# Kernel optimization log

Measured on AMD Instinct MI355X. Metric: run time of the kernel, lower is better.

The kernel has to match this reference:

```python
import jax, jax.numpy as jnp
import numpy as np

PADDING = 1
STRIDE = 1

def setup_inputs() -> dict:
    key = jax.random.key(0)
    k1, k2 = jax.random.split(key)
    x = jax.random.normal(k1, (32, 64, 64, 64), dtype=jnp.float32)
    # kaiming_normal fan_out, relu: std = sqrt(2 / (out_ch * k * k))
    fan_out = 128 * 3 * 3
    std = np.sqrt(2.0 / fan_out).astype(np.float32)
    weight = jax.random.normal(k2, (128, 64, 3, 3), dtype=jnp.float32) * std
    bias = jnp.zeros((128,), dtype=jnp.float32)
    return {"x": x, "weight": weight, "bias": bias}

def reference(x, weight, bias):
    # Faithful to the unfold+multiply+sum path, which computes a standard
    # cross-correlation conv2d (torch conv semantics) with stride/padding.
    out = jax.lax.conv_general_dilated(
        x, weight,
        window_strides=(STRIDE, STRIDE),
        padding=[(PADDING, PADDING), (PADDING, PADDING)],
        dimension_numbers=("NCHW", "OIHW", "NCHW"),
    )
    return out + bias[None, :, None, None]
```

## Files before the change

kernel.cpp:

```cpp
#include <hip/hip_runtime.h>


typedef short short8 __attribute__((ext_vector_type(8)));
typedef float f32x4  __attribute__((ext_vector_type(4)));

static __device__ __forceinline__ unsigned short f2bf(float f) {
    unsigned int u = __float_as_uint(f);
    u = (u + 0x7FFFu + ((u >> 16) & 1u)) >> 16;
    return (unsigned short)u;
}
static __device__ __forceinline__ unsigned int pk2(float lo, float hi) {
    return (unsigned int)f2bf(lo) | ((unsigned int)f2bf(hi) << 16);
}

__global__ __launch_bounds__(256)
void prep_x(const float* __restrict__ x, unsigned short* __restrict__ xT)
{
    __shared__ float T[64][65];
    const int h = blockIdx.x, n = blockIdx.y, tid = threadIdx.x;
    const size_t nbase = (size_t)n * 262144 + (size_t)h * 64;
    #pragma unroll
    for (int i = 0; i < 16; ++i) {
        int idx = tid + i * 256;
        int ci = idx >> 6, w = idx & 63;
        T[ci][w] = x[nbase + (size_t)ci * 4096 + w];
    }
    __syncthreads();
    const int w = tid >> 2, cg = tid & 3;
    unsigned int pk[8];
    #pragma unroll
    for (int k = 0; k < 8; ++k)
        pk[k] = pk2(T[cg * 16 + 2 * k][w], T[cg * 16 + 2 * k + 1][w]);
    unsigned short* dst = xT + (((size_t)n * 64 + h) * 64 + w) * 64 + cg * 16;
    uint4 a; a.x = pk[0]; a.y = pk[1]; a.z = pk[2]; a.w = pk[3];
    uint4 b; b.x = pk[4]; b.y = pk[5]; b.z = pk[6]; b.w = pk[7];
    *(uint4*)(dst)     = a;
    *(uint4*)(dst + 8) = b;
}

__global__ __launch_bounds__(256)
void prep_w(const float* __restrict__ w, unsigned short* __restrict__ wT)
{
    int t = blockIdx.x * 256 + threadIdx.x;
    if (t >= 128 * 576) return;
    int co = t / 576, r = t - co * 576;
    int p = r >> 6, ci = r & 63;
    wT[t] = f2bf(w[(size_t)(co * 64 + ci) * 9 + p]);
}

#define XBUF 50688
#define WBUF 8192
#define TOTAL_LDS (XBUF + 2*WBUF)

__global__ __launch_bounds__(256, 2)
void conv_mfma3(const unsigned short* __restrict__ xT,
                const unsigned short* __restrict__ wT,
                const float* __restrict__ bias,
                float* __restrict__ out)
{
    extern __shared__ __align__(16) char lds[];
    char* wl = lds + XBUF;

    const int tid  = threadIdx.x;
    const int cb   = blockIdx.x;
    const int h0   = blockIdx.y * 4;
    const int n    = blockIdx.z;
    const int wrow = tid >> 6;
    const int lane = tid & 63;
    const int l15  = lane & 15, l4 = lane >> 4;

    const unsigned short* xTn = xT + (size_t)n * 262144;
    const unsigned short* wTb = wT + (size_t)cb * 64 * 576;

    const int wco = tid >> 3, wg = tid & 7;
    const int wds0 = wco * 128 + ((wg ^ (wco & 7)) * 16);
    const int wds1 = wds0 + 32 * 128;
    const unsigned short* wsrc0 = wTb + wco * 576 + wg * 8;
    const unsigned short* wsrc1 = wTb + (wco + 32) * 576 + wg * 8;

    f32x4 breg[4];
    #pragma unroll
    for (int mf = 0; mf < 4; ++mf)
        breg[mf] = *(const f32x4*)(bias + cb * 64 + mf * 16 + l4 * 4);

    {
        uint4 xreg[13];
        #pragma unroll
        for (int k = 0; k < 13; ++k) {
            int G = tid + k * 256;
            if (k < 12 || tid < 96) {
                int hp = G / 528, rem = G - hp * 528;
                int wp = rem >> 3, g = rem & 7;
                int gh = h0 + hp - 1, gw = wp - 1;
                uint4 v; v.x = v.y = v.z = v.w = 0u;
                if ((unsigned)gh < 64u && (unsigned)gw < 64u)
                    v = *(const uint4*)(xTn + ((gh * 64 + gw) * 64 + g * 8));
                xreg[k] = v;
            }
        }
        uint4 w0a = *(const uint4*)(wsrc0);
        uint4 w0b = *(const uint4*)(wsrc1);
        #pragma unroll
        for (int k = 0; k < 13; ++k) {
            int G = tid + k * 256;
            if (k < 12 || tid < 96) {
                int hp = G / 528, rem = G - hp * 528;
                int wp = rem >> 3, g = rem & 7;
                *(uint4*)(lds + (hp * 66 + wp) * 128 + ((g ^ (wp & 7)) * 16)) = xreg[k];
            }
        }
        *(uint4*)(wl + wds0) = w0a;
        *(uint4*)(wl + wds1) = w0b;
    }
    __syncthreads();

    f32x4 acc[4][4];
    #pragma unroll
    for (int mf = 0; mf < 4; ++mf)
        #pragma unroll
        for (int nf = 0; nf < 4; ++nf)
            acc[mf][nf] = (f32x4)0.0f;

    #pragma unroll
    for (int p = 0; p < 9; ++p) {
        const char* wbr = wl + ((p & 1) ? WBUF : 0);
        char*       wbw = wl + ((p & 1) ? 0 : WBUF);
        const int kh = p / 3, kw = p - kh * 3;

        uint4 nw0, nw1;
        if (p < 8) {
            nw0 = *(const uint4*)(wsrc0 + (p + 1) * 64);
            nw1 = *(const uint4*)(wsrc1 + (p + 1) * 64);
        }

        #pragma unroll
        for (int c = 0; c < 2; ++c) {
            short8 Af[4], Bf[4];
            #pragma unroll
            for (int mf = 0; mf < 4; ++mf) {
                const int co = mf * 16 + l15;
                Af[mf] = *(const short8*)(wbr + co * 128 + (((c * 4 + l4) ^ (co & 7)) * 16));
            }
            #pragma unroll
            for (int nf = 0; nf < 4; ++nf) {
                const int hp = wrow + kh;
                const int wp = nf * 16 + l15 + kw;
                Bf[nf] = *(const short8*)(lds + (hp * 66 + wp) * 128 + (((c * 4 + l4) ^ (wp & 7)) * 16));
            }
            #pragma unroll
            for (int mf = 0; mf < 4; ++mf)
                #pragma unroll
                for (int nf = 0; nf < 4; ++nf)
                    acc[mf][nf] = __builtin_amdgcn_mfma_f32_16x16x32_bf16(
                        Af[mf], Bf[nf], acc[mf][nf], 0, 0, 0);
        }

        if (p < 8) {
            *(uint4*)(wbw + wds0) = nw0;
            *(uint4*)(wbw + wds1) = nw1;
            __syncthreads();
        }
    }

    {
        const int h = h0 + wrow;
        #pragma unroll
        for (int mf = 0; mf < 4; ++mf) {
            #pragma unroll
            for (int r = 0; r < 4; ++r) {
                const int co = cb * 64 + mf * 16 + l4 * 4 + r;
                float* orow = out + (((size_t)n * 128 + co) * 64 + h) * 64;
                const float bv = breg[mf][r];
                #pragma unroll
                for (int nf = 0; nf < 4; ++nf)
                    orow[nf * 16 + l15] = acc[mf][nf][r] + bv;
            }
        }
    }
}

__global__ __launch_bounds__(256, 4)
void conv2d_f32_tiled(const float* __restrict__ x,
                      const float* __restrict__ wgt,
                      const float* __restrict__ bias,
                      float* __restrict__ out)
{
    __shared__ float Xlds[8][10][66];
    __shared__ float Wlds[32][72];
    const int tid = threadIdx.x;
    const int co0 = blockIdx.x * 32, h0 = blockIdx.y * 8, n = blockIdx.z;
    const int tco = tid >> 6, lane = tid & 63;
    float acc[8][8];
    #pragma unroll
    for (int i = 0; i < 8; ++i)
        #pragma unroll
        for (int j = 0; j < 8; ++j) acc[i][j] = 0.0f;
    for (int cc = 0; cc < 8; ++cc) {
        const int ci0 = cc * 8;
        for (int idx = tid; idx < 8 * 10 * 66; idx += 256) {
            const int ww = idx % 66, t = idx / 66, hh = t % 10, ci = t / 10;
            const int gh = h0 + hh - 1, gw = ww - 1;
            float v = 0.0f;
            if ((unsigned)gh < 64u && (unsigned)gw < 64u)
                v = x[(((size_t)n * 64 + ci0 + ci) * 64 + gh) * 64 + gw];
            Xlds[ci][hh][ww] = v;
        }
        for (int idx = tid; idx < 32 * 72; idx += 256) {
            const int r = idx % 72, co = idx / 72;
            Wlds[co][r] = wgt[(size_t)(co0 + co) * 576 + ci0 * 9 + r];
        }
        __syncthreads();
        for (int ci = 0; ci < 8; ++ci)
            #pragma unroll
            for (int kh = 0; kh < 3; ++kh)
                #pragma unroll
                for (int kw = 0; kw < 3; ++kw) {
                    float wv[8];
                    #pragma unroll
                    for (int i = 0; i < 8; ++i) wv[i] = Wlds[tco * 8 + i][ci * 9 + kh * 3 + kw];
                    #pragma unroll
                    for (int j = 0; j < 8; ++j) {
                        const float xv = Xlds[ci][j + kh][lane + kw];
                        #pragma unroll
                        for (int i = 0; i < 8; ++i) acc[i][j] = fmaf(wv[i], xv, acc[i][j]);
                    }
                }
        __syncthreads();
    }
    #pragma unroll
    for (int i = 0; i < 8; ++i) {
        const int co = co0 + tco * 8 + i;
        const float b = bias[co];
        #pragma unroll
        for (int j = 0; j < 8; ++j)
            out[(((size_t)n * 128 + co) * 64 + (h0 + j)) * 64 + lane] = acc[i][j] + b;
    }
}

extern "C" void kernel_launch(void* const* d_in, const int* in_sizes, int n_in,
                              void* d_out, int out_size, void* d_ws, size_t ws_size,
                              hipStream_t stream)
{
    const float* x    = (const float*)d_in[0];
    const float* wgt  = (const float*)d_in[1];
    const float* bias = (const float*)d_in[2];
    float* out        = (float*)d_out;

    const size_t XT_BYTES = (size_t)32 * 64 * 64 * 64 * 2;
    const size_t WT_BYTES = (size_t)128 * 576 * 2;

    if (ws_size < XT_BYTES + WT_BYTES) {
        dim3 grid(4, 8, 32);
        conv2d_f32_tiled<<<grid, 256, 0, stream>>>(x, wgt, bias, out);
        return;
    }

    unsigned short* xT = (unsigned short*)d_ws;
    unsigned short* wT = (unsigned short*)((char*)d_ws + XT_BYTES);

    (void)hipFuncSetAttribute((const void*)conv_mfma3,
                              hipFuncAttributeMaxDynamicSharedMemorySize, TOTAL_LDS);

    prep_x<<<dim3(64, 32), 256, 0, stream>>>(x, xT);
    prep_w<<<dim3((128 * 576 + 255) / 256), 256, 0, stream>>>(wgt, wT);
    conv_mfma3<<<dim3(2, 16, 32), 256, TOTAL_LDS, stream>>>(xT, wT, bias, out);
}
```

Baseline: 44.73 us.

## Pre-swizzle weights into MFMA fragment layout and load A directly from global

The weight prep kernel now writes bf16 weights in the exact per-lane MFMA A-fragment order, so the conv kernel loads A fragments straight from global memory (L2/L1 cached) instead of staging them through double-buffered LDS. This removes the weight LDS buffers, the per-tap weight stores and the eight per-tap __syncthreads. The lower LDS footprint lets launch bounds ask for three blocks per CU instead of two. The cost is that weight fragments come from global/cache on every tap, which adds latency and cache traffic in the inner loop.

```diff
diff --git a/kernel.cpp b/kernel.cpp
--- a/kernel.cpp
+++ b/kernel.cpp
@@ -39,27 +39,29 @@
 }
 
 __global__ __launch_bounds__(256)
-void prep_w(const float* __restrict__ w, unsigned short* __restrict__ wT)
+void prep_w(const float* __restrict__ w, unsigned short* __restrict__ wA)
 {
     int t = blockIdx.x * 256 + threadIdx.x;
-    if (t >= 128 * 576) return;
-    int co = t / 576, r = t - co * 576;
-    int p = r >> 6, ci = r & 63;
-    wT[t] = f2bf(w[(size_t)(co * 64 + ci) * 9 + p]);
-}
-
-#define XBUF 50688
-#define WBUF 8192
-#define TOTAL_LDS (XBUF + 2*WBUF)
-
-__global__ __launch_bounds__(256, 2)
-void conv_mfma3(const unsigned short* __restrict__ xT,
-                const unsigned short* __restrict__ wT,
+    if (t >= 73728) return;
+    int j    = t & 7;
+    int lane = (t >> 3) & 63;
+    int mf   = (t >> 9) & 3;
+    int c    = (t >> 11) & 1;
+    int rest = t >> 12;
+    int p    = rest % 9;
+    int cb   = rest / 9;
+    int co = cb * 64 + mf * 16 + (lane & 15);
+    int ci = c * 32 + (lane >> 4) * 8 + j;
+    wA[t] = f2bf(w[(size_t)(co * 64 + ci) * 9 + p]);
+}
+
+__global__ __launch_bounds__(256, 3)
+void conv_mfma4(const unsigned short* __restrict__ xT,
+                const unsigned short* __restrict__ wA,
                 const float* __restrict__ bias,
                 float* __restrict__ out)
 {
-    extern __shared__ __align__(16) char lds[];
-    char* wl = lds + XBUF;
+    __shared__ __align__(16) char lds[50688];
 
     const int tid  = threadIdx.x;
     const int cb   = blockIdx.x;
@@ -70,13 +72,7 @@
     const int l15  = lane & 15, l4 = lane >> 4;
 
     const unsigned short* xTn = xT + (size_t)n * 262144;
-    const unsigned short* wTb = wT + (size_t)cb * 64 * 576;
-
-    const int wco = tid >> 3, wg = tid & 7;
-    const int wds0 = wco * 128 + ((wg ^ (wco & 7)) * 16);
-    const int wds1 = wds0 + 32 * 128;
-    const unsigned short* wsrc0 = wTb + wco * 576 + wg * 8;
-    const unsigned short* wsrc1 = wTb + (wco + 32) * 576 + wg * 8;
+    const unsigned short* wAb = wA + (size_t)cb * 36864;
 
     f32x4 breg[4];
     #pragma unroll
@@ -98,8 +94,6 @@
                 xreg[k] = v;
             }
         }
-        uint4 w0a = *(const uint4*)(wsrc0);
-        uint4 w0b = *(const uint4*)(wsrc1);
         #pragma unroll
         for (int k = 0; k < 13; ++k) {
             int G = tid + k * 256;
@@ -109,8 +103,6 @@
                 *(uint4*)(lds + (hp * 66 + wp) * 128 + ((g ^ (wp & 7)) * 16)) = xreg[k];
             }
         }
-        *(uint4*)(wl + wds0) = w0a;
-        *(uint4*)(wl + wds1) = w0b;
     }
     __syncthreads();
 
@@ -123,24 +115,13 @@
 
     #pragma unroll
     for (int p = 0; p < 9; ++p) {
-        const char* wbr = wl + ((p & 1) ? WBUF : 0);
-        char*       wbw = wl + ((p & 1) ? 0 : WBUF);
         const int kh = p / 3, kw = p - kh * 3;
-
-        uint4 nw0, nw1;
-        if (p < 8) {
-            nw0 = *(const uint4*)(wsrc0 + (p + 1) * 64);
-            nw1 = *(const uint4*)(wsrc1 + (p + 1) * 64);
-        }
-
         #pragma unroll
         for (int c = 0; c < 2; ++c) {
             short8 Af[4], Bf[4];
             #pragma unroll
-            for (int mf = 0; mf < 4; ++mf) {
-                const int co = mf * 16 + l15;
-                Af[mf] = *(const short8*)(wbr + co * 128 + (((c * 4 + l4) ^ (co & 7)) * 16));
-            }
+            for (int mf = 0; mf < 4; ++mf)
+                Af[mf] = *(const short8*)(wAb + ((((p * 2 + c) * 4 + mf) * 64 + lane) << 3));
             #pragma unroll
             for (int nf = 0; nf < 4; ++nf) {
                 const int hp = wrow + kh;
@@ -153,12 +134,6 @@
                 for (int nf = 0; nf < 4; ++nf)
                     acc[mf][nf] = __builtin_amdgcn_mfma_f32_16x16x32_bf16(
                         Af[mf], Bf[nf], acc[mf][nf], 0, 0, 0);
-        }
-
-        if (p < 8) {
-            *(uint4*)(wbw + wds0) = nw0;
-            *(uint4*)(wbw + wds1) = nw1;
-            __syncthreads();
         }
     }
 
@@ -256,12 +231,9 @@
     }
 
     unsigned short* xT = (unsigned short*)d_ws;
-    unsigned short* wT = (unsigned short*)((char*)d_ws + XT_BYTES);
-
-    (void)hipFuncSetAttribute((const void*)conv_mfma3,
-                              hipFuncAttributeMaxDynamicSharedMemorySize, TOTAL_LDS);
+    unsigned short* wA = (unsigned short*)((char*)d_ws + XT_BYTES);
 
     prep_x<<<dim3(64, 32), 256, 0, stream>>>(x, xT);
-    prep_w<<<dim3((128 * 576 + 255) / 256), 256, 0, stream>>>(wgt, wT);
-    conv_mfma3<<<dim3(2, 16, 32), 256, TOTAL_LDS, stream>>>(xT, wT, bias, out);
-}
+    prep_w<<<dim3((73728 + 255) / 256), 256, 0, stream>>>(wgt, wA);
+    conv_mfma4<<<dim3(2, 16, 32), 256, 0, stream>>>(xT, wA, bias, out);
+}
```

Result: slower. 46.70 us (+4.4%).
